# Optimization experiments

Hardware: AMD Instinct MI355X
Metric: run time of the kernel (lower is better)

The kernel has to match this reference:

```python
import jax, jax.numpy as jnp
import numpy as np
from jax import lax

H = W = 128          # feature map size (gen_line_map uses 128x128)
C = 128              # dim_loi
NPTS0 = 32           # n_pts0 samples per line
NPTS1 = 8            # after MaxPool1d(4, stride=4)
TOPK = 50            # n_dyn_junc
SCALE = 5.0          # proposal_lines distance scale


def proposal_lines(md_maps, dis_maps, scale=SCALE):
    h, w = md_maps.shape[1], md_maps.shape[2]
    y0, x0 = jnp.meshgrid(jnp.arange(h, dtype=jnp.float32),
                          jnp.arange(w, dtype=jnp.float32), indexing='ij')
    md_ = (md_maps[0] - 0.5) * np.pi * 2
    st_ = md_maps[1] * np.pi / 2
    ed_ = -md_maps[2] * np.pi / 2
    cs_md, ss_md = jnp.cos(md_), jnp.sin(md_)
    cs_st = jnp.clip(jnp.cos(st_), 0.001, None)
    ss_st = jnp.clip(jnp.sin(st_), 0.001, None)
    cs_ed = jnp.clip(jnp.cos(ed_), 0.001, None)
    ss_ed = jnp.clip(jnp.sin(ed_), None, -0.001)
    y_st = ss_st / cs_st
    y_ed = ss_ed / cs_ed
    d = dis_maps[0] * scale
    x_st = (cs_md - ss_md * y_st) * d
    y_s = (ss_md + cs_md * y_st) * d
    x_ed = (cs_md - ss_md * y_ed) * d
    y_e = (ss_md + cs_md * y_ed) * d
    x_st_f = jnp.clip(x_st + x0, 0.0, w - 1)
    y_st_f = jnp.clip(y_s + y0, 0.0, h - 1)
    x_ed_f = jnp.clip(x_ed + x0, 0.0, w - 1)
    y_ed_f = jnp.clip(y_e + y0, 0.0, h - 1)
    return jnp.stack((x_st_f, y_st_f, x_ed_f, y_ed_f), axis=-1).reshape(-1, 4)


def pooling(feats, lines):
    # feats: [C, H, W]; lines: [N, 4]
    h, w = feats.shape[1], feats.shape[2]
    tspan = jnp.linspace(0.0, 1.0, NPTS0)[None, None, :]           # [1,1,32]
    U, V = lines[:, :2], lines[:, 2:]
    sp = U[:, :, None] * tspan + V[:, :, None] * (1 - tspan) - 0.5  # [N,2,32]
    sp = sp.transpose(0, 2, 1).reshape(-1, 2)                       # [N*32, 2]
    px, py = sp[:, 0], sp[:, 1]
    px0 = jnp.clip(jnp.floor(px), 0.0, w - 1)
    py0 = jnp.clip(jnp.floor(py), 0.0, h - 1)
    px1 = jnp.clip(px0 + 1, 0.0, w - 1)
    py1 = jnp.clip(py0 + 1, 0.0, h - 1)
    px0l, py0l = px0.astype(jnp.int32), py0.astype(jnp.int32)
    px1l, py1l = px1.astype(jnp.int32), py1.astype(jnp.int32)
    # bilinear gather-weight, fused in a single expression: [C, N*32]
    xp = (feats[:, py0l, px0l] * (py1 - py) * (px1 - px)
          + feats[:, py1l, px0l] * (py - py0) * (px1 - px)
          + feats[:, py0l, px1l] * (py1 - py) * (px - px0)
          + feats[:, py1l, px1l] * (py - py0) * (px - px0))
    xp = xp.reshape(C, -1, NPTS0).transpose(1, 0, 2)                # [N, C, 32]
    xp = xp.reshape(xp.shape[0], C, NPTS1, NPTS0 // NPTS1).max(-1)  # MaxPool1d(4,4)
    return xp.reshape(-1, NPTS1 * C)                                # [N, 1024]


def nms(a):
    # F.max_pool2d(a, 3, stride=1, padding=1) then keep local maxima
    ap = lax.reduce_window(a, -jnp.inf, lax.max, (1, 3, 3), (1, 1, 1), 'SAME')
    return a * (a == ap).astype(a.dtype)


def get_junctions(jloc_nms, joff, topk=TOPK):
    h, w = jloc_nms.shape[1], jloc_nms.shape[2]
    scores, index = lax.top_k(jloc_nms.reshape(-1), topk)
    jf = joff.reshape(2, -1)
    y = (index // w).astype(jnp.float32) + jf[1][index] + 0.5
    x = (index % w).astype(jnp.float32) + jf[0][index] + 0.5
    juncs = jnp.stack((x, y), axis=1)                               # [topk, 2]
    return juncs, scores, index


def setup_inputs() -> dict:
    key = jax.random.key(0)
    ks = jax.random.split(key, 12)
    return {
        'md': jax.random.uniform(ks[0], (3, H, W), dtype=jnp.float32),
        'dis': jax.random.uniform(ks[1], (1, H, W), dtype=jnp.float32),
        'res': jax.random.uniform(ks[2], (1, H, W), dtype=jnp.float32),
        'jloc': jax.random.uniform(ks[3], (1, H, W), dtype=jnp.float32),
        'joff': jax.random.uniform(ks[4], (2, H, W), dtype=jnp.float32) - 0.5,
        'feats': jax.random.normal(ks[5], (C, H, W), dtype=jnp.float32),
        'W1': jax.random.normal(ks[6], (1024, C * NPTS1), dtype=jnp.float32) * 0.02,
        'b1': jax.random.normal(ks[7], (1024,), dtype=jnp.float32) * 0.02,
        'W2': jax.random.normal(ks[8], (1024, 1024), dtype=jnp.float32) * 0.02,
        'b2': jax.random.normal(ks[9], (1024,), dtype=jnp.float32) * 0.02,
        'W3': jax.random.normal(ks[10], (1, 1024), dtype=jnp.float32) * 0.02,
        'b3': jax.random.normal(ks[11], (1,), dtype=jnp.float32) * 0.02,
    }


def reference(md, dis, res, jloc, joff, feats, W1, b1, W2, b2, W3, b3):
    # line proposals at 3 residual scales (use_residual=True)
    lines = jnp.concatenate([
        proposal_lines(md, dis + s * res) for s in (-1.0, 0.0, 1.0)
    ], axis=0)                                                      # [3*H*W, 4]
    # LOI bilinear pooling + scoring MLP (self.fc)
    x = pooling(feats, lines)                                       # [N, 1024]
    x = jax.nn.relu(x @ W1.T + b1)
    x = jax.nn.relu(x @ W2.T + b2)
    logits = x @ W3.T + b3                                          # [N, 1]
    # junction decode: NMS + topk + offset gather
    juncs, jscores, _ = get_junctions(nms(jloc), joff, TOPK)
    return logits, juncs, jscores
```

## Files before the change

### kernel.cpp

```cpp
#include <hip/hip_runtime.h>
#include <hip/hip_bf16.h>
#include <math.h>

#define HH 128
#define WW 128
#define HW 16384
#define NL 49152
#define CC 128
#define NPTS0 32
#define NPTS1 8
#define PI_F 3.14159265358979323846f

typedef __attribute__((ext_vector_type(8))) short short8;
typedef __attribute__((ext_vector_type(4))) float f32x4;

__device__ __forceinline__ ushort f2bf(float f) {
    unsigned u = __builtin_bit_cast(unsigned, f);
    unsigned rounding = 0x7FFFu + ((u >> 16) & 1u);
    return (ushort)((u + rounding) >> 16);
}

__device__ __forceinline__ void gload_lds16(const void* gsrc, void* ldst) {
    __builtin_amdgcn_global_load_lds(
        (const __attribute__((address_space(1))) unsigned int*)gsrc,
        (__attribute__((address_space(3))) unsigned int*)ldst,
        16, 0, 0);
}

__device__ __forceinline__ void unpk8(uint4 d, float* f) {
    f[0] = __builtin_bit_cast(float, d.x << 16);
    f[1] = __builtin_bit_cast(float, d.x & 0xFFFF0000u);
    f[2] = __builtin_bit_cast(float, d.y << 16);
    f[3] = __builtin_bit_cast(float, d.y & 0xFFFF0000u);
    f[4] = __builtin_bit_cast(float, d.z << 16);
    f[5] = __builtin_bit_cast(float, d.z & 0xFFFF0000u);
    f[6] = __builtin_bit_cast(float, d.w << 16);
    f[7] = __builtin_bit_cast(float, d.w & 0xFFFF0000u);
}

__global__ __launch_bounds__(256) void k_lines(
    const float* __restrict__ md, const float* __restrict__ dis,
    const float* __restrict__ res, float* __restrict__ lines)
{
    int g = blockIdx.x * 256 + threadIdx.x;
    if (g >= NL) return;
    int s = g / HW;
    int pix = g - s * HW;
    float sf = (float)(s - 1);
    int y = pix >> 7, x = pix & 127;

    float md0 = md[pix], md1 = md[HW + pix], md2 = md[2 * HW + pix];
    float d = (dis[pix] + sf * res[pix]) * 5.0f;

    float md_ = (md0 - 0.5f) * (2.0f * PI_F);
    float st_ = md1 * (0.5f * PI_F);
    float ed_ = -md2 * (0.5f * PI_F);
    float cs_md = cosf(md_), ss_md = sinf(md_);
    float cs_st = fmaxf(cosf(st_), 0.001f);
    float ss_st = fmaxf(sinf(st_), 0.001f);
    float cs_ed = fmaxf(cosf(ed_), 0.001f);
    float ss_ed = fminf(sinf(ed_), -0.001f);
    float y_st = ss_st / cs_st;
    float y_ed = ss_ed / cs_ed;
    float x_st = (cs_md - ss_md * y_st) * d;
    float y_s  = (ss_md + cs_md * y_st) * d;
    float x_ed = (cs_md - ss_md * y_ed) * d;
    float y_e  = (ss_md + cs_md * y_ed) * d;

    float4 o;
    o.x = fminf(fmaxf(x_st + (float)x, 0.0f), 127.0f);
    o.y = fminf(fmaxf(y_s  + (float)y, 0.0f), 127.0f);
    o.z = fminf(fmaxf(x_ed + (float)x, 0.0f), 127.0f);
    o.w = fminf(fmaxf(y_e  + (float)y, 0.0f), 127.0f);
    ((float4*)lines)[g] = o;
}

__global__ void k_transpose(const float* __restrict__ in, ushort* __restrict__ out)
{
    __shared__ float tile[32][33];
    int cb = blockIdx.x;
    int pb = blockIdx.y;
    int tx = threadIdx.x, ty = threadIdx.y;
#pragma unroll
    for (int j = 0; j < 32; j += 8)
        tile[ty + j][tx] = in[(size_t)(cb * 32 + ty + j) * HW + pb * 32 + tx];
    __syncthreads();
#pragma unroll
    for (int j = 0; j < 32; j += 8)
        out[(size_t)(pb * 32 + ty + j) * CC + cb * 32 + tx] = f2bf(tile[tx][ty + j]);
}

__global__ void k_cvt(const float* __restrict__ a, const float* __restrict__ b,
                      ushort* __restrict__ oa, ushort* __restrict__ ob, int n)
{
    int i = blockIdx.x * 256 + threadIdx.x;
    if (i < n) { oa[i] = f2bf(a[i]); ob[i] = f2bf(b[i]); }
}

__global__ __launch_bounds__(128, 4) void k_pool(
    const ushort* __restrict__ ft, const float* __restrict__ lines,
    ushort* __restrict__ X)
{
    __shared__ __align__(16) unsigned smeta[2048];
    const int t = threadIdx.x;
    const int l_loc = t >> 4, c8 = t & 15;
    const int gl0 = blockIdx.x * 8;

#pragma unroll
    for (int e = 0; e < 2; ++e) {
        int s = t + e * 128;
        int ml = s >> 5, sp = s & 31;
        float4 L = ((const float4*)lines)[gl0 + ml];
        float tf = (float)sp * (1.0f / 31.0f);
        float omt = 1.0f - tf;
        float px = L.x * tf + L.z * omt - 0.5f;
        float py = L.y * tf + L.w * omt - 0.5f;
        float px0 = fminf(fmaxf(floorf(px), 0.0f), 127.0f);
        float py0 = fminf(fmaxf(floorf(py), 0.0f), 127.0f);
        float px1 = fminf(px0 + 1.0f, 127.0f);
        float py1 = fminf(py0 + 1.0f, 127.0f);
        int ix0 = (int)px0, iy0 = (int)py0, ix1 = (int)px1, iy1 = (int)py1;
        float4 wv;
        wv.x = (py1 - py) * (px1 - px);
        wv.y = (py  - py0) * (px1 - px);
        wv.z = (py1 - py) * (px  - px0);
        wv.w = (py  - py0) * (px  - px0);
        int o00 = (iy0 * WW + ix0) * (CC * 2);
        int dx  = (ix1 - ix0) * (CC * 2);
        int dy  = (iy1 - iy0) * (WW * CC * 2);
        int4 ov;
        ov.x = o00;
        ov.y = o00 + dy;
        ov.z = o00 + dx;
        ov.w = o00 + dy + dx;
        *(float4*)&smeta[s * 8]     = wv;
        *(int4*)  &smeta[s * 8 + 4] = ov;
    }
    __syncthreads();

    const unsigned coff = (unsigned)(c8 * 16);
    const char* fbase = (const char*)ft;
    float m[8][8];
#pragma unroll
    for (int ch = 0; ch < 8; ++ch)
#pragma unroll
        for (int g = 0; g < 8; ++g) m[ch][g] = -INFINITY;

#pragma unroll
    for (int g = 0; g < 8; ++g) {
#pragma unroll
        for (int j = 0; j < 4; ++j) {
            const unsigned* mp = &smeta[(l_loc * 32 + g * 4 + j) * 8];
            float4 wv = *(const float4*)mp;
            int4  ov = *(const int4*)(mp + 4);
            uint4 d00 = *(const uint4*)(fbase + ((unsigned)ov.x + coff));
            uint4 d10 = *(const uint4*)(fbase + ((unsigned)ov.y + coff));
            uint4 d01 = *(const uint4*)(fbase + ((unsigned)ov.z + coff));
            uint4 d11 = *(const uint4*)(fbase + ((unsigned)ov.w + coff));
            float f00[8], f10[8], f01[8], f11[8];
            unpk8(d00, f00); unpk8(d10, f10); unpk8(d01, f01); unpk8(d11, f11);
#pragma unroll
            for (int ch = 0; ch < 8; ++ch) {
                float v = f00[ch] * wv.x + f10[ch] * wv.y
                        + f01[ch] * wv.z + f11[ch] * wv.w;
                m[ch][g] = fmaxf(m[ch][g], v);
            }
        }
    }

    ushort* Xp = X + (size_t)(gl0 + l_loc) * 1024 + c8 * 64;
#pragma unroll
    for (int ch = 0; ch < 8; ++ch) {
        short8 pk;
#pragma unroll
        for (int g = 0; g < 8; ++g) pk[g] = (short)f2bf(m[ch][g]);
        *(short8*)(Xp + ch * 8) = pk;
    }
}

#define NT 32
template<int EPI>
__global__ __launch_bounds__(512, 2) void k_gemm2(
    const ushort* __restrict__ A, const ushort* __restrict__ B,
    const float* __restrict__ bias, ushort* __restrict__ Y,
    const float* __restrict__ w3, float* __restrict__ logits,
    int M, int N, int K)
{
    __shared__ __align__(16) ushort lds[65536];
    const int tid = threadIdx.x;
    const int w = tid >> 6, l = tid & 63;
    const int lr = l & 15, kq = l >> 4;
    const int wm = w >> 2, wn = w & 3;

    const int nwg = gridDim.x;
    const int cpx = nwg >> 3;
    const int swz = (blockIdx.x & 7) * cpx + (blockIdx.x >> 3);
    const int nbm = M >> 8;
    const int m_blk = swz % nbm;
    const int n_blk = swz / nbm;
    const int m0 = m_blk << 8, n0 = n_blk << 8;

    const int G0 = tid, G1 = 512 + tid;
    const int r0 = G0 >> 2, r1 = G1 >> 2;
    const int g0 = (G0 & 3) ^ ((r0 >> 1) & 3);
    const int g1 = (G1 & 3) ^ ((r1 >> 1) & 3);
    const ushort* sA0 = A + (size_t)(m0 + r0) * K + g0 * 8;
    const ushort* sA1 = A + (size_t)(m0 + r1) * K + g1 * 8;
    const ushort* sB0 = B + (size_t)(n0 + r0) * K + g0 * 8;
    const ushort* sB1 = B + (size_t)(n0 + r1) * K + g1 * 8;
    ushort* dA0 = &lds[G0 * 8];
    ushort* dA1 = &lds[G1 * 8];
    ushort* dB0 = &lds[32768 + G0 * 8];
    ushort* dB1 = &lds[32768 + G1 * 8];

#define STAGE_A(tp) { int sb_ = ((tp) & 3) * 8192; \
    gload_lds16(sA0 + (tp) * 32, dA0 + sb_); \
    gload_lds16(sA1 + (tp) * 32, dA1 + sb_); }
#define STAGE_B(tp) { int sb_ = ((tp) & 3) * 8192; \
    gload_lds16(sB0 + (tp) * 32, dB0 + sb_); \
    gload_lds16(sB1 + (tp) * 32, dB1 + sb_); }
#define SBAR  { __builtin_amdgcn_sched_barrier(0); __builtin_amdgcn_s_barrier(); \
                __builtin_amdgcn_sched_barrier(0); }

    int aidx[8], bidx[4];
#pragma unroll
    for (int m = 0; m < 8; ++m) {
        int r = wm * 128 + m * 16 + lr;
        int g = kq ^ ((r >> 1) & 3);
        aidx[m] = r * 32 + g * 8;
    }
#pragma unroll
    for (int n = 0; n < 4; ++n) {
        int r = wn * 64 + n * 16 + lr;
        int g = kq ^ ((r >> 1) & 3);
        bidx[n] = 32768 + r * 32 + g * 8;
    }

    f32x4 acc[8][4] = {};

    STAGE_A(0); STAGE_B(0); STAGE_A(1); STAGE_B(1); STAGE_A(2);
    asm volatile("s_waitcnt vmcnt(6)" ::: "memory");
    SBAR;

    for (int t = 0; t < NT; ++t) {
        const int sb = (t & 3) * 8192;
        short8 bq0 = *(const short8*)&lds[sb + bidx[0]];
        short8 bq1 = *(const short8*)&lds[sb + bidx[1]];
        short8 bq2 = *(const short8*)&lds[sb + bidx[2]];
        short8 bq3 = *(const short8*)&lds[sb + bidx[3]];
        short8 a[8];
#pragma unroll
        for (int m = 0; m < 8; ++m)
            a[m] = *(const short8*)&lds[sb + aidx[m]];
        if (t + 2 < NT) STAGE_B(t + 2);
        if (t + 3 < NT) STAGE_A(t + 3);
        __builtin_amdgcn_s_setprio(1);
#pragma unroll
        for (int m = 0; m < 8; ++m) {
            acc[m][0] = __builtin_amdgcn_mfma_f32_16x16x32_bf16(bq0, a[m], acc[m][0], 0, 0, 0);
            acc[m][1] = __builtin_amdgcn_mfma_f32_16x16x32_bf16(bq1, a[m], acc[m][1], 0, 0, 0);
            acc[m][2] = __builtin_amdgcn_mfma_f32_16x16x32_bf16(bq2, a[m], acc[m][2], 0, 0, 0);
            acc[m][3] = __builtin_amdgcn_mfma_f32_16x16x32_bf16(bq3, a[m], acc[m][3], 0, 0, 0);
        }
        __builtin_amdgcn_s_setprio(0);
        if (t < NT - 3) {
            asm volatile("s_waitcnt vmcnt(6)" ::: "memory");
        } else {
            asm volatile("s_waitcnt vmcnt(0)" ::: "memory");
        }
        SBAR;
    }
#undef STAGE_A
#undef STAGE_B
#undef SBAR

    if (EPI == 0) {
#pragma unroll
        for (int n = 0; n < 4; ++n) {
            int cbase = n0 + wn * 64 + n * 16 + kq * 4;
            float4 bv4 = *(const float4*)&bias[cbase];
#pragma unroll
            for (int m = 0; m < 8; ++m) {
                int row = m0 + wm * 128 + m * 16 + lr;
                ushort4 pk;
                pk.x = f2bf(fmaxf(acc[m][n][0] + bv4.x, 0.0f));
                pk.y = f2bf(fmaxf(acc[m][n][1] + bv4.y, 0.0f));
                pk.z = f2bf(fmaxf(acc[m][n][2] + bv4.z, 0.0f));
                pk.w = f2bf(fmaxf(acc[m][n][3] + bv4.w, 0.0f));
                *(ushort4*)(Y + (size_t)row * N + cbase) = pk;
            }
        }
    } else {
        float4 bv4[4], w34[4];
#pragma unroll
        for (int n = 0; n < 4; ++n) {
            int cbase = n0 + wn * 64 + n * 16 + kq * 4;
            bv4[n] = *(const float4*)&bias[cbase];
            w34[n] = *(const float4*)&w3[cbase];
        }
#pragma unroll
        for (int m = 0; m < 8; ++m) {
            float s = 0.0f;
#pragma unroll
            for (int n = 0; n < 4; ++n) {
                s += fmaxf(acc[m][n][0] + bv4[n].x, 0.0f) * w34[n].x;
                s += fmaxf(acc[m][n][1] + bv4[n].y, 0.0f) * w34[n].y;
                s += fmaxf(acc[m][n][2] + bv4[n].z, 0.0f) * w34[n].z;
                s += fmaxf(acc[m][n][3] + bv4[n].w, 0.0f) * w34[n].w;
            }
            s += __shfl_xor(s, 16, 64);
            s += __shfl_xor(s, 32, 64);
            if (kq == 0)
                atomicAdd(&logits[m0 + wm * 128 + m * 16 + lr], s);
        }
    }
}

__global__ void k_init_logits(float* __restrict__ logits, const float* __restrict__ b3, int n)
{
    int i = blockIdx.x * 256 + threadIdx.x;
    if (i < n) logits[i] = b3[0];
}

__global__ __launch_bounds__(256) void k_nms_topk(
    const float* __restrict__ jloc, unsigned long long* __restrict__ cand)
{
    __shared__ unsigned long long sk[256];
    const int t = threadIdx.x;
    const int idx = blockIdx.x * 256 + t;
    const int y = idx >> 7, x = idx & 127;
    float cv = jloc[idx];
    float m = cv;
    for (int dy = -1; dy <= 1; ++dy) {
        int yy = y + dy;
        if (yy < 0 || yy > 127) continue;
        for (int dx = -1; dx <= 1; ++dx) {
            int xx = x + dx;
            if (xx < 0 || xx > 127) continue;
            m = fmaxf(m, jloc[(yy << 7) + xx]);
        }
    }
    float nv = (cv == m) ? cv : 0.0f;
    unsigned vb = __builtin_bit_cast(unsigned, nv);
    sk[t] = ((unsigned long long)vb << 32) | (unsigned)(0xFFFFFFFFu - idx);
    __syncthreads();
    for (int k = 2; k <= 256; k <<= 1) {
        for (int j = k >> 1; j >= 1; j >>= 1) {
            int ixj = t ^ j;
            if (ixj > t) {
                unsigned long long a = sk[t], b = sk[ixj];
                bool up = ((t & k) == 0);
                if (up ? (a < b) : (a > b)) { sk[t] = b; sk[ixj] = a; }
            }
            __syncthreads();
        }
    }
    if (t < 64) cand[blockIdx.x * 64 + t] = (t < 50) ? sk[t] : 0ull;
}

__global__ __launch_bounds__(1024) void k_topk_final(
    const unsigned long long* __restrict__ cand,
    const float* __restrict__ joff, float* __restrict__ outj)
{
    __shared__ unsigned long long sk[4096];
    const int t = threadIdx.x;
#pragma unroll
    for (int e = 0; e < 4; ++e) sk[t + (e << 10)] = cand[t + (e << 10)];
    __syncthreads();
    for (int k = 2; k <= 4096; k <<= 1) {
        for (int j = k >> 1; j >= 1; j >>= 1) {
#pragma unroll
            for (int e = 0; e < 4; ++e) {
                int i = t + (e << 10);
                int ixj = i ^ j;
                if (ixj > i) {
                    unsigned long long a = sk[i], b = sk[ixj];
                    bool up = ((i & k) == 0);
                    if (up ? (a < b) : (a > b)) { sk[i] = b; sk[ixj] = a; }
                }
            }
            __syncthreads();
        }
    }
    if (t < 50) {
        unsigned long long kk = sk[t];
        unsigned idx = 0xFFFFFFFFu - (unsigned)(kk & 0xFFFFFFFFull);
        float val = __builtin_bit_cast(float, (unsigned)(kk >> 32));
        int y = idx >> 7, x = idx & 127;
        outj[2 * t]     = (float)x + joff[idx]      + 0.5f;
        outj[2 * t + 1] = (float)y + joff[HW + idx] + 0.5f;
        outj[100 + t]   = val;
    }
}

extern "C" void kernel_launch(void* const* d_in, const int* in_sizes, int n_in,
                              void* d_out, int out_size, void* d_ws, size_t ws_size,
                              hipStream_t stream) {
    const float* md   = (const float*)d_in[0];
    const float* dis  = (const float*)d_in[1];
    const float* res  = (const float*)d_in[2];
    const float* jloc = (const float*)d_in[3];
    const float* joff = (const float*)d_in[4];
    const float* feats= (const float*)d_in[5];
    const float* W1   = (const float*)d_in[6];
    const float* b1   = (const float*)d_in[7];
    const float* W2   = (const float*)d_in[8];
    const float* b2   = (const float*)d_in[9];
    const float* W3   = (const float*)d_in[10];
    const float* b3   = (const float*)d_in[11];
    float* out = (float*)d_out;

    char* ws = (char*)d_ws;
    size_t off = 0;
    auto alloc = [&](size_t bytes) {
        void* p = ws + off;
        off = (off + bytes + 255) & ~(size_t)255;
        return p;
    };
    float*  lines = (float*) alloc((size_t)NL * 4 * sizeof(float));
    ushort* ft    = (ushort*)alloc((size_t)HW * CC * 2);
    ushort* W1b   = (ushort*)alloc((size_t)1024 * 1024 * 2);
    ushort* W2b   = (ushort*)alloc((size_t)1024 * 1024 * 2);
    ushort* X     = (ushort*)alloc((size_t)NL * 1024 * 2);
    ushort* Y1    = (ushort*)alloc((size_t)NL * 1024 * 2);
    unsigned long long* cand = (unsigned long long*)alloc(4096 * 8);

    k_lines<<<NL / 256, 256, 0, stream>>>(md, dis, res, lines);
    k_transpose<<<dim3(CC / 32, HW / 32), dim3(32, 8), 0, stream>>>(feats, ft);
    k_cvt<<<(1024 * 1024) / 256, 256, 0, stream>>>(W1, W2, W1b, W2b, 1024 * 1024);
    k_pool<<<NL / 8, 128, 0, stream>>>(ft, lines, X);

    int ngrid = (NL / 256) * (1024 / 256);
    k_gemm2<0><<<ngrid, 512, 0, stream>>>(X, W1b, b1, Y1, nullptr, nullptr, NL, 1024, 1024);
    k_init_logits<<<NL / 256, 256, 0, stream>>>(out, b3, NL);
    k_gemm2<1><<<ngrid, 512, 0, stream>>>(Y1, W2b, b2, nullptr, W3, out, NL, 1024, 1024);

    k_nms_topk<<<64, 256, 0, stream>>>(jloc, cand);
    k_topk_final<<<1, 1024, 0, stream>>>(cand, joff, out + NL);
}
```

Measured before the change: 370.4 us.

## Split GEMM main loop into interleaved MFMA clusters with staggered wave order

Restructures the GEMM K-loop so the A fragments are loaded from LDS and consumed in two clusters of four M-rows, with global-to-LDS staging of B and A interleaved between the clusters. Odd and even waves run the clusters in opposite order to spread LDS read pressure. Prefetch depth for A drops from three stages to two, and the vmcnt waits change to match. This aims to cut register pressure and improve overlap of memory issue with MFMA work, but the shallower prefetch may expose more global load latency.

```diff
diff --git a/kernel.cpp b/kernel.cpp
--- a/kernel.cpp
+++ b/kernel.cpp
@@ -237,10 +237,35 @@
     }
 
     f32x4 acc[8][4] = {};
-
-    STAGE_A(0); STAGE_B(0); STAGE_A(1); STAGE_B(1); STAGE_A(2);
-    asm volatile("s_waitcnt vmcnt(6)" ::: "memory");
+    const bool wodd = (w & 1) != 0;
+
+    STAGE_A(0); STAGE_B(0); STAGE_A(1); STAGE_B(1);
+    asm volatile("s_waitcnt vmcnt(4)" ::: "memory");
     SBAR;
+
+#define CLUSTER(mlo) { \
+    short8 am0 = *(const short8*)&lds[sb + aidx[(mlo)]];     \
+    short8 am1 = *(const short8*)&lds[sb + aidx[(mlo) + 1]]; \
+    short8 am2 = *(const short8*)&lds[sb + aidx[(mlo) + 2]]; \
+    short8 am3 = *(const short8*)&lds[sb + aidx[(mlo) + 3]]; \
+    __builtin_amdgcn_s_setprio(1);                            \
+    acc[(mlo)][0]   = __builtin_amdgcn_mfma_f32_16x16x32_bf16(bq0, am0, acc[(mlo)][0], 0, 0, 0);   \
+    acc[(mlo)][1]   = __builtin_amdgcn_mfma_f32_16x16x32_bf16(bq1, am0, acc[(mlo)][1], 0, 0, 0);   \
+    acc[(mlo)][2]   = __builtin_amdgcn_mfma_f32_16x16x32_bf16(bq2, am0, acc[(mlo)][2], 0, 0, 0);   \
+    acc[(mlo)][3]   = __builtin_amdgcn_mfma_f32_16x16x32_bf16(bq3, am0, acc[(mlo)][3], 0, 0, 0);   \
+    acc[(mlo)+1][0] = __builtin_amdgcn_mfma_f32_16x16x32_bf16(bq0, am1, acc[(mlo)+1][0], 0, 0, 0); \
+    acc[(mlo)+1][1] = __builtin_amdgcn_mfma_f32_16x16x32_bf16(bq1, am1, acc[(mlo)+1][1], 0, 0, 0); \
+    acc[(mlo)+1][2] = __builtin_amdgcn_mfma_f32_16x16x32_bf16(bq2, am1, acc[(mlo)+1][2], 0, 0, 0); \
+    acc[(mlo)+1][3] = __builtin_amdgcn_mfma_f32_16x16x32_bf16(bq3, am1, acc[(mlo)+1][3], 0, 0, 0); \
+    acc[(mlo)+2][0] = __builtin_amdgcn_mfma_f32_16x16x32_bf16(bq0, am2, acc[(mlo)+2][0], 0, 0, 0); \
+    acc[(mlo)+2][1] = __builtin_amdgcn_mfma_f32_16x16x32_bf16(bq1, am2, acc[(mlo)+2][1], 0, 0, 0); \
+    acc[(mlo)+2][2] = __builtin_amdgcn_mfma_f32_16x16x32_bf16(bq2, am2, acc[(mlo)+2][2], 0, 0, 0); \
+    acc[(mlo)+2][3] = __builtin_amdgcn_mfma_f32_16x16x32_bf16(bq3, am2, acc[(mlo)+2][3], 0, 0, 0); \
+    acc[(mlo)+3][0] = __builtin_amdgcn_mfma_f32_16x16x32_bf16(bq0, am3, acc[(mlo)+3][0], 0, 0, 0); \
+    acc[(mlo)+3][1] = __builtin_amdgcn_mfma_f32_16x16x32_bf16(bq1, am3, acc[(mlo)+3][1], 0, 0, 0); \
+    acc[(mlo)+3][2] = __builtin_amdgcn_mfma_f32_16x16x32_bf16(bq2, am3, acc[(mlo)+3][2], 0, 0, 0); \
+    acc[(mlo)+3][3] = __builtin_amdgcn_mfma_f32_16x16x32_bf16(bq3, am3, acc[(mlo)+3][3], 0, 0, 0); \
+    __builtin_amdgcn_s_setprio(0); }
 
     for (int t = 0; t < NT; ++t) {
         const int sb = (t & 3) * 8192;
@@ -248,28 +273,25 @@
         short8 bq1 = *(const short8*)&lds[sb + bidx[1]];
         short8 bq2 = *(const short8*)&lds[sb + bidx[2]];
         short8 bq3 = *(const short8*)&lds[sb + bidx[3]];
-        short8 a[8];
-#pragma unroll
-        for (int m = 0; m < 8; ++m)
-            a[m] = *(const short8*)&lds[sb + aidx[m]];
-        if (t + 2 < NT) STAGE_B(t + 2);
-        if (t + 3 < NT) STAGE_A(t + 3);
-        __builtin_amdgcn_s_setprio(1);
-#pragma unroll
-        for (int m = 0; m < 8; ++m) {
-            acc[m][0] = __builtin_amdgcn_mfma_f32_16x16x32_bf16(bq0, a[m], acc[m][0], 0, 0, 0);
-            acc[m][1] = __builtin_amdgcn_mfma_f32_16x16x32_bf16(bq1, a[m], acc[m][1], 0, 0, 0);
-            acc[m][2] = __builtin_amdgcn_mfma_f32_16x16x32_bf16(bq2, a[m], acc[m][2], 0, 0, 0);
-            acc[m][3] = __builtin_amdgcn_mfma_f32_16x16x32_bf16(bq3, a[m], acc[m][3], 0, 0, 0);
-        }
-        __builtin_amdgcn_s_setprio(0);
-        if (t < NT - 3) {
-            asm volatile("s_waitcnt vmcnt(6)" ::: "memory");
+        if (wodd) {
+            CLUSTER(4)
+            if (t + 2 < NT) STAGE_B(t + 2);
+            CLUSTER(0)
+            if (t + 2 < NT) STAGE_A(t + 2);
+        } else {
+            CLUSTER(0)
+            if (t + 2 < NT) STAGE_B(t + 2);
+            CLUSTER(4)
+            if (t + 2 < NT) STAGE_A(t + 2);
+        }
+        if (t < NT - 2) {
+            asm volatile("s_waitcnt vmcnt(4)" ::: "memory");
         } else {
             asm volatile("s_waitcnt vmcnt(0)" ::: "memory");
         }
         SBAR;
     }
+#undef CLUSTER
 #undef STAGE_A
 #undef STAGE_B
 #undef SBAR
```

Result: no change. 371.5 us (+0.3%).

## Restructure GEMM mainloop to 64-wide K tiles with 8-phase interleaved prefetch

Applied to the files above, without the earlier changes.

Rewrites the bf16 MFMA GEMM main loop to stage 64-wide K tiles into two LDS ping-pong halves, with an 8-way XOR swizzle. Each iteration is split into eight phases, and each phase issues one global-to-LDS prefetch slice alongside a batch of 16 MFMAs between barriers. This is meant to hide memory latency more evenly and lower per-K-step barrier overhead. Launch bounds drop from two blocks per CU to one, which gives up occupancy for more registers. The extra barriers per iteration add sync cost.

```diff
diff --git a/kernel.cpp b/kernel.cpp
--- a/kernel.cpp
+++ b/kernel.cpp
@@ -178,9 +178,9 @@
     }
 }
 
-#define NT 32
+#define NIT 8
 template<int EPI>
-__global__ __launch_bounds__(512, 2) void k_gemm2(
+__global__ __launch_bounds__(512, 1) void k_gemm2(
     const ushort* __restrict__ A, const ushort* __restrict__ B,
     const float* __restrict__ bias, ushort* __restrict__ Y,
     const float* __restrict__ w3, float* __restrict__ logits,
@@ -194,85 +194,171 @@
 
     const int nwg = gridDim.x;
     const int cpx = nwg >> 3;
-    const int swz = (blockIdx.x & 7) * cpx + (blockIdx.x >> 3);
+    const int swzb = (blockIdx.x & 7) * cpx + (blockIdx.x >> 3);
     const int nbm = M >> 8;
-    const int m_blk = swz % nbm;
-    const int n_blk = swz / nbm;
+    const int m_blk = swzb % nbm;
+    const int n_blk = swzb / nbm;
     const int m0 = m_blk << 8, n0 = n_blk << 8;
 
-    const int G0 = tid, G1 = 512 + tid;
-    const int r0 = G0 >> 2, r1 = G1 >> 2;
-    const int g0 = (G0 & 3) ^ ((r0 >> 1) & 3);
-    const int g1 = (G1 & 3) ^ ((r1 >> 1) & 3);
-    const ushort* sA0 = A + (size_t)(m0 + r0) * K + g0 * 8;
-    const ushort* sA1 = A + (size_t)(m0 + r1) * K + g1 * 8;
-    const ushort* sB0 = B + (size_t)(n0 + r0) * K + g0 * 8;
-    const ushort* sB1 = B + (size_t)(n0 + r1) * K + g1 * 8;
-    ushort* dA0 = &lds[G0 * 8];
-    ushort* dA1 = &lds[G1 * 8];
-    ushort* dB0 = &lds[32768 + G0 * 8];
-    ushort* dB1 = &lds[32768 + G1 * 8];
-
-#define STAGE_A(tp) { int sb_ = ((tp) & 3) * 8192; \
-    gload_lds16(sA0 + (tp) * 32, dA0 + sb_); \
-    gload_lds16(sA1 + (tp) * 32, dA1 + sb_); }
-#define STAGE_B(tp) { int sb_ = ((tp) & 3) * 8192; \
-    gload_lds16(sB0 + (tp) * 32, dB0 + sb_); \
-    gload_lds16(sB1 + (tp) * 32, dB1 + sb_); }
-#define SBAR  { __builtin_amdgcn_sched_barrier(0); __builtin_amdgcn_s_barrier(); \
-                __builtin_amdgcn_sched_barrier(0); }
-
-    int aidx[8], bidx[4];
-#pragma unroll
-    for (int m = 0; m < 8; ++m) {
-        int r = wm * 128 + m * 16 + lr;
-        int g = kq ^ ((r >> 1) & 3);
-        aidx[m] = r * 32 + g * 8;
-    }
-#pragma unroll
-    for (int n = 0; n < 4; ++n) {
-        int r = wn * 64 + n * 16 + lr;
-        int g = kq ^ ((r >> 1) & 3);
-        bidx[n] = 32768 + r * 32 + g * 8;
-    }
+    const ushort* pA = A + (size_t)m0 * K;
+    const ushort* pB = B + (size_t)n0 * K;
+
+    const int rS = tid >> 3;
+    const int gS = (tid & 7) ^ (rS & 7);
+
+#define STG(gp, rowoff, kt, regbase) { \
+    gload_lds16((gp) + (size_t)((rowoff) + rS) * K + (kt) * 64 + gS * 8, \
+                &lds[(regbase) + tid * 8]); \
+    gload_lds16((gp) + (size_t)((rowoff) + 64 + rS) * K + (kt) * 64 + gS * 8, \
+                &lds[(regbase) + 4096 + tid * 8]); }
+
+#define FBAR { __builtin_amdgcn_sched_barrier(0); __builtin_amdgcn_s_barrier(); \
+               __builtin_amdgcn_sched_barrier(0); }
+
+    const int swz0 = ((kq) ^ (lr & 7)) * 8;
+    const int swz1 = ((4 + kq) ^ (lr & 7)) * 8;
+    int aoff[8], boff[4];
+#pragma unroll
+    for (int m = 0; m < 8; ++m) aoff[m] = (wm * 128 + m * 16 + lr) * 64;
+#pragma unroll
+    for (int n = 0; n < 4; ++n) boff[n] = 16384 + (wn * 64 + n * 16 + lr) * 64;
 
     f32x4 acc[8][4] = {};
-
-    STAGE_A(0); STAGE_B(0); STAGE_A(1); STAGE_B(1); STAGE_A(2);
-    asm volatile("s_waitcnt vmcnt(6)" ::: "memory");
-    SBAR;
-
-    for (int t = 0; t < NT; ++t) {
-        const int sb = (t & 3) * 8192;
-        short8 bq0 = *(const short8*)&lds[sb + bidx[0]];
-        short8 bq1 = *(const short8*)&lds[sb + bidx[1]];
-        short8 bq2 = *(const short8*)&lds[sb + bidx[2]];
-        short8 bq3 = *(const short8*)&lds[sb + bidx[3]];
-        short8 a[8];
-#pragma unroll
-        for (int m = 0; m < 8; ++m)
-            a[m] = *(const short8*)&lds[sb + aidx[m]];
-        if (t + 2 < NT) STAGE_B(t + 2);
-        if (t + 3 < NT) STAGE_A(t + 3);
-        __builtin_amdgcn_s_setprio(1);
-#pragma unroll
-        for (int m = 0; m < 8; ++m) {
-            acc[m][0] = __builtin_amdgcn_mfma_f32_16x16x32_bf16(bq0, a[m], acc[m][0], 0, 0, 0);
-            acc[m][1] = __builtin_amdgcn_mfma_f32_16x16x32_bf16(bq1, a[m], acc[m][1], 0, 0, 0);
-            acc[m][2] = __builtin_amdgcn_mfma_f32_16x16x32_bf16(bq2, a[m], acc[m][2], 0, 0, 0);
-            acc[m][3] = __builtin_amdgcn_mfma_f32_16x16x32_bf16(bq3, a[m], acc[m][3], 0, 0, 0);
-        }
-        __builtin_amdgcn_s_setprio(0);
-        if (t < NT - 3) {
-            asm volatile("s_waitcnt vmcnt(6)" ::: "memory");
-        } else {
-            asm volatile("s_waitcnt vmcnt(0)" ::: "memory");
-        }
-        SBAR;
-    }
-#undef STAGE_A
-#undef STAGE_B
-#undef SBAR
+    short8 bq0, bq1, bq2, bq3;
+
+#define MF16(MLO, A0, A1, A2, A3) \
+    acc[MLO+0][0] = __builtin_amdgcn_mfma_f32_16x16x32_bf16(bq0, A0, acc[MLO+0][0], 0, 0, 0); \
+    acc[MLO+0][1] = __builtin_amdgcn_mfma_f32_16x16x32_bf16(bq1, A0, acc[MLO+0][1], 0, 0, 0); \
+    acc[MLO+0][2] = __builtin_amdgcn_mfma_f32_16x16x32_bf16(bq2, A0, acc[MLO+0][2], 0, 0, 0); \
+    acc[MLO+0][3] = __builtin_amdgcn_mfma_f32_16x16x32_bf16(bq3, A0, acc[MLO+0][3], 0, 0, 0); \
+    acc[MLO+1][0] = __builtin_amdgcn_mfma_f32_16x16x32_bf16(bq0, A1, acc[MLO+1][0], 0, 0, 0); \
+    acc[MLO+1][1] = __builtin_amdgcn_mfma_f32_16x16x32_bf16(bq1, A1, acc[MLO+1][1], 0, 0, 0); \
+    acc[MLO+1][2] = __builtin_amdgcn_mfma_f32_16x16x32_bf16(bq2, A1, acc[MLO+1][2], 0, 0, 0); \
+    acc[MLO+1][3] = __builtin_amdgcn_mfma_f32_16x16x32_bf16(bq3, A1, acc[MLO+1][3], 0, 0, 0); \
+    acc[MLO+2][0] = __builtin_amdgcn_mfma_f32_16x16x32_bf16(bq0, A2, acc[MLO+2][0], 0, 0, 0); \
+    acc[MLO+2][1] = __builtin_amdgcn_mfma_f32_16x16x32_bf16(bq1, A2, acc[MLO+2][1], 0, 0, 0); \
+    acc[MLO+2][2] = __builtin_amdgcn_mfma_f32_16x16x32_bf16(bq2, A2, acc[MLO+2][2], 0, 0, 0); \
+    acc[MLO+2][3] = __builtin_amdgcn_mfma_f32_16x16x32_bf16(bq3, A2, acc[MLO+2][3], 0, 0, 0); \
+    acc[MLO+3][0] = __builtin_amdgcn_mfma_f32_16x16x32_bf16(bq0, A3, acc[MLO+3][0], 0, 0, 0); \
+    acc[MLO+3][1] = __builtin_amdgcn_mfma_f32_16x16x32_bf16(bq1, A3, acc[MLO+3][1], 0, 0, 0); \
+    acc[MLO+3][2] = __builtin_amdgcn_mfma_f32_16x16x32_bf16(bq2, A3, acc[MLO+3][2], 0, 0, 0); \
+    acc[MLO+3][3] = __builtin_amdgcn_mfma_f32_16x16x32_bf16(bq3, A3, acc[MLO+3][3], 0, 0, 0);
+
+    STG(pA, 0,   0, 0);
+    STG(pA, 128, 0, 8192);
+    STG(pB, 0,   0, 16384);
+    STG(pB, 128, 0, 24576);
+    STG(pB, 0,   1, 49152);
+    asm volatile("s_waitcnt vmcnt(2)" ::: "memory");
+    FBAR;
+
+    for (int i = 0; i < NIT; ++i) {
+        const int t1 = 2 * i + 1, t2 = 2 * i + 2, t3 = 2 * i + 3;
+        const bool pf = (i < NIT - 1);
+
+        bq0 = *(const short8*)&lds[boff[0] + swz0];
+        bq1 = *(const short8*)&lds[boff[1] + swz0];
+        bq2 = *(const short8*)&lds[boff[2] + swz0];
+        bq3 = *(const short8*)&lds[boff[3] + swz0];
+        {
+            short8 a0 = *(const short8*)&lds[aoff[0] + swz0];
+            short8 a1 = *(const short8*)&lds[aoff[1] + swz0];
+            short8 a2 = *(const short8*)&lds[aoff[2] + swz0];
+            short8 a3 = *(const short8*)&lds[aoff[3] + swz0];
+            STG(pB, 128, t1, 57344);
+            FBAR;
+            __builtin_amdgcn_s_setprio(1); MF16(0, a0, a1, a2, a3) __builtin_amdgcn_s_setprio(0);
+            FBAR;
+        }
+        {
+            short8 a4 = *(const short8*)&lds[aoff[4] + swz0];
+            short8 a5 = *(const short8*)&lds[aoff[5] + swz0];
+            short8 a6 = *(const short8*)&lds[aoff[6] + swz0];
+            short8 a7 = *(const short8*)&lds[aoff[7] + swz0];
+            STG(pA, 0, t1, 32768);
+            FBAR;
+            __builtin_amdgcn_s_setprio(1); MF16(4, a4, a5, a6, a7) __builtin_amdgcn_s_setprio(0);
+            FBAR;
+        }
+        bq0 = *(const short8*)&lds[boff[0] + swz1];
+        bq1 = *(const short8*)&lds[boff[1] + swz1];
+        bq2 = *(const short8*)&lds[boff[2] + swz1];
+        bq3 = *(const short8*)&lds[boff[3] + swz1];
+        {
+            short8 a0 = *(const short8*)&lds[aoff[0] + swz1];
+            short8 a1 = *(const short8*)&lds[aoff[1] + swz1];
+            short8 a2 = *(const short8*)&lds[aoff[2] + swz1];
+            short8 a3 = *(const short8*)&lds[aoff[3] + swz1];
+            STG(pA, 128, t1, 40960);
+            FBAR;
+            __builtin_amdgcn_s_setprio(1); MF16(0, a0, a1, a2, a3) __builtin_amdgcn_s_setprio(0);
+            FBAR;
+        }
+        {
+            short8 a4 = *(const short8*)&lds[aoff[4] + swz1];
+            short8 a5 = *(const short8*)&lds[aoff[5] + swz1];
+            short8 a6 = *(const short8*)&lds[aoff[6] + swz1];
+            short8 a7 = *(const short8*)&lds[aoff[7] + swz1];
+            if (pf) STG(pB, 0, t2, 16384);
+            FBAR;
+            __builtin_amdgcn_s_setprio(1); MF16(4, a4, a5, a6, a7) __builtin_amdgcn_s_setprio(0);
+            if (pf) { asm volatile("s_waitcnt vmcnt(2)" ::: "memory"); }
+            else    { asm volatile("s_waitcnt vmcnt(0)" ::: "memory"); }
+            FBAR;
+        }
+        bq0 = *(const short8*)&lds[32768 + boff[0] + swz0];
+        bq1 = *(const short8*)&lds[32768 + boff[1] + swz0];
+        bq2 = *(const short8*)&lds[32768 + boff[2] + swz0];
+        bq3 = *(const short8*)&lds[32768 + boff[3] + swz0];
+        {
+            short8 a0 = *(const short8*)&lds[32768 + aoff[0] + swz0];
+            short8 a1 = *(const short8*)&lds[32768 + aoff[1] + swz0];
+            short8 a2 = *(const short8*)&lds[32768 + aoff[2] + swz0];
+            short8 a3 = *(const short8*)&lds[32768 + aoff[3] + swz0];
+            if (pf) STG(pB, 128, t2, 24576);
+            FBAR;
+            __builtin_amdgcn_s_setprio(1); MF16(0, a0, a1, a2, a3) __builtin_amdgcn_s_setprio(0);
+            FBAR;
+        }
+        {
+            short8 a4 = *(const short8*)&lds[32768 + aoff[4] + swz0];
+            short8 a5 = *(const short8*)&lds[32768 + aoff[5] + swz0];
+            short8 a6 = *(const short8*)&lds[32768 + aoff[6] + swz0];
+            short8 a7 = *(const short8*)&lds[32768 + aoff[7] + swz0];
+            if (pf) STG(pA, 0, t2, 0);
+            FBAR;
+            __builtin_amdgcn_s_setprio(1); MF16(4, a4, a5, a6, a7) __builtin_amdgcn_s_setprio(0);
+            FBAR;
+        }
+        bq0 = *(const short8*)&lds[32768 + boff[0] + swz1];
+        bq1 = *(const short8*)&lds[32768 + boff[1] + swz1];
+        bq2 = *(const short8*)&lds[32768 + boff[2] + swz1];
+        bq3 = *(const short8*)&lds[32768 + boff[3] + swz1];
+        {
+            short8 a0 = *(const short8*)&lds[32768 + aoff[0] + swz1];
+            short8 a1 = *(const short8*)&lds[32768 + aoff[1] + swz1];
+            short8 a2 = *(const short8*)&lds[32768 + aoff[2] + swz1];
+            short8 a3 = *(const short8*)&lds[32768 + aoff[3] + swz1];
+            if (pf) STG(pA, 128, t2, 8192);
+            FBAR;
+            __builtin_amdgcn_s_setprio(1); MF16(0, a0, a1, a2, a3) __builtin_amdgcn_s_setprio(0);
+            FBAR;
+        }
+        {
+            short8 a4 = *(const short8*)&lds[32768 + aoff[4] + swz1];
+            short8 a5 = *(const short8*)&lds[32768 + aoff[5] + swz1];
+            short8 a6 = *(const short8*)&lds[32768 + aoff[6] + swz1];
+            short8 a7 = *(const short8*)&lds[32768 + aoff[7] + swz1];
+            if (pf) STG(pB, 0, t3, 49152);
+            FBAR;
+            __builtin_amdgcn_s_setprio(1); MF16(4, a4, a5, a6, a7) __builtin_amdgcn_s_setprio(0);
+            if (pf) { asm volatile("s_waitcnt vmcnt(2)" ::: "memory"); }
+            FBAR;
+        }
+    }
+#undef STG
+#undef FBAR
+#undef MF16
 
     if (EPI == 0) {
 #pragma unroll
```

New measurement: 352.8 us. -4.7%, faster.
